# Kernel optimization log

Hardware: AMD Instinct MI355X
Metric: run time of the kernel (lower is better)

The kernel has to match this reference:

```python
import jax, jax.numpy as jnp
import numpy as np

B, C_IN, IMG, P = 32, 3, 224, 16
D, H, L, F, NCLS = 768, 12, 12, 3072, 1000
NP = IMG // P          # 14 patches per side
S = NP * NP + 1        # 197 tokens (cls + patches)
DH = D // H            # 64 head dim
EPS = 1e-5


def _ln(x, g, b):
    m = jnp.mean(x, axis=-1, keepdims=True)
    v = jnp.mean(jnp.square(x - m), axis=-1, keepdims=True)
    return (x - m) * jax.lax.rsqrt(v + EPS) * g + b


def setup_inputs() -> dict:
    key = jax.random.key(0)
    ks = iter(jax.random.split(key, 32))
    w = lambda shape: jax.random.normal(next(ks), shape, dtype=jnp.float32) * 0.02
    inp = {
        "X": jax.random.normal(next(ks), (B, C_IN, IMG, IMG), dtype=jnp.float32),
        "patch_w": w((D, C_IN, P, P)),
        "patch_b": jnp.zeros((D,), jnp.float32),
        "cls_token": w((1, 1, D)),
        "pos_emb": w((1, S, D)),
        # per-layer stacked params; linear weights stored [in, out]
        "ln1_g": jnp.ones((L, D), jnp.float32), "ln1_b": jnp.zeros((L, D), jnp.float32),
        "Wq": w((L, D, D)), "bq": jnp.zeros((L, D), jnp.float32),
        "Wk": w((L, D, D)), "bk": jnp.zeros((L, D), jnp.float32),
        "Wv": w((L, D, D)), "bv": jnp.zeros((L, D), jnp.float32),
        "Wo": w((L, D, D)), "bo": jnp.zeros((L, D), jnp.float32),
        "ln2_g": jnp.ones((L, D), jnp.float32), "ln2_b": jnp.zeros((L, D), jnp.float32),
        "Wf1": w((L, D, F)), "bf1": jnp.zeros((L, F), jnp.float32),
        "Wf2": w((L, F, D)), "bf2": jnp.zeros((L, D), jnp.float32),
        "lnf_g": jnp.ones((D,), jnp.float32), "lnf_b": jnp.zeros((D,), jnp.float32),
        "head_w": w((D, NCLS)), "head_b": jnp.zeros((NCLS,), jnp.float32),
    }
    return inp


def _vit(X, patch_w, patch_b, cls_token, pos_emb,
         ln1_g, ln1_b, Wq, bq, Wk, bk, Wv, bv, Wo, bo,
         ln2_g, ln2_b, Wf1, bf1, Wf2, bf2, lnf_g, lnf_b, head_w, head_b):
    # patch embed: stride==kernel conv as block-reshape + einsum
    xb = X.reshape(B, C_IN, NP, P, NP, P)
    patches = jnp.einsum('bchpwq,dcpq->bhwd', xb, patch_w).reshape(B, NP * NP, D) + patch_b
    x = jnp.concatenate([jnp.broadcast_to(cls_token, (B, 1, D)), patches], axis=1)
    x = x + pos_emb  # [B, S, D]

    scale = 1.0 / jnp.sqrt(jnp.float32(DH))

    def block(x, p):
        g1, b1, wq, bq_, wk, bk_, wv, bv_, wo, bo_, g2, b2, w1, b1f, w2, b2f = p
        h = _ln(x, g1, b1)
        q = (h @ wq + bq_).reshape(B, S, H, DH)
        k = (h @ wk + bk_).reshape(B, S, H, DH)
        v = (h @ wv + bv_).reshape(B, S, H, DH)
        scores = jnp.einsum('bshd,bthd->bhst', q, k) * scale
        probs = jax.nn.softmax(scores, axis=-1)
        attn = jnp.einsum('bhst,bthd->bshd', probs, v).reshape(B, S, D)
        x = x + attn @ wo + bo_
        h = _ln(x, g2, b2)
        x = x + jax.nn.gelu(h @ w1 + b1f, approximate=False) @ w2 + b2f
        return x, None

    layers = (ln1_g, ln1_b, Wq, bq, Wk, bk, Wv, bv, Wo, bo,
              ln2_g, ln2_b, Wf1, bf1, Wf2, bf2)
    x, _ = jax.lax.scan(block, x, layers)

    x = _ln(x, lnf_g, lnf_b)
    return x[:, 0] @ head_w + head_b  # [B, NCLS]


def reference(X, patch_w, patch_b, cls_token, pos_emb,
              ln1_g, ln1_b, Wq, bq, Wk, bk, Wv, bv, Wo, bo,
              ln2_g, ln2_b, Wf1, bf1, Wf2, bf2, lnf_g, lnf_b, head_w, head_b):
    return _vit(X, patch_w, patch_b, cls_token, pos_emb,
                ln1_g, ln1_b, Wq, bq, Wk, bk, Wv, bv, Wo, bo,
                ln2_g, ln2_b, Wf1, bf1, Wf2, bf2, lnf_g, lnf_b, head_w, head_b)
```

## Files before the change

kernel.cpp:

```cpp
#include <hip/hip_runtime.h>
#include <math.h>

#define Bn 32
#define Sn 197
#define Dn 768
#define Hn 12
#define DHn 64
#define Fn 3072
#define Ln 12
#define NPATCH 196
#define NCLSn 1000
#define MTOK (Bn * Sn)
#define MPAD 6400

typedef __attribute__((ext_vector_type(8))) short short8;
typedef __attribute__((ext_vector_type(4))) float f32x4;

__device__ __forceinline__ unsigned short f2bf(float f) {
  union { float f; unsigned int u; } v; v.f = f;
  unsigned int r = v.u + 0x7fffu + ((v.u >> 16) & 1u);
  return (unsigned short)(r >> 16);
}
__device__ __forceinline__ float bf2f(unsigned short h) {
  union { unsigned int u; float f; } v; v.u = ((unsigned int)h) << 16;
  return v.f;
}

__device__ __forceinline__ void gload16(const unsigned short* g, unsigned short* l) {
  __builtin_amdgcn_global_load_lds(
      (const __attribute__((address_space(1))) unsigned int*)g,
      (__attribute__((address_space(3))) unsigned int*)l, 16, 0, 0);
}

__global__ __launch_bounds__(256) void transpose_cast(
    const float* __restrict__ in, unsigned short* __restrict__ out,
    int rows, int cols) {
  __shared__ float tile[32][33];
  int c0 = blockIdx.x * 32, r0 = blockIdx.y * 32;
  int tx = threadIdx.x, ty = threadIdx.y;
  for (int i = 0; i < 32; i += 8) {
    int r = r0 + ty + i, c = c0 + tx;
    tile[ty + i][tx] = (r < rows && c < cols) ? in[(size_t)r * cols + c] : 0.f;
  }
  __syncthreads();
  for (int i = 0; i < 32; i += 8) {
    int c = c0 + ty + i, r = r0 + tx;
    if (c < cols && r < rows)
      out[(size_t)c * rows + r] = f2bf(tile[tx][ty + i]);
  }
}

__global__ __launch_bounds__(256) void cast_bf(
    const float* __restrict__ in, unsigned short* __restrict__ out, int n) {
  int i = blockIdx.x * 256 + threadIdx.x;
  if (i < n) out[i] = f2bf(in[i]);
}

__global__ __launch_bounds__(256) void im2col_patches(
    const float* __restrict__ X, unsigned short* __restrict__ A) {
  int idx = blockIdx.x * 256 + threadIdx.x;
  if (idx >= NPATCH * Bn * Dn) return;
  int col = idx % Dn, row = idx / Dn;
  int b = row / NPATCH, pi = row % NPATCH;
  int hp = pi / 14, wp = pi % 14;
  int c = col >> 8, r2 = col & 255, p = r2 >> 4, q = r2 & 15;
  A[idx] = f2bf(X[(((size_t)b * 3 + c) * 224 + hp * 16 + p) * 224 + wp * 16 + q]);
}

__global__ __launch_bounds__(256) void init_cls(
    const float* __restrict__ cls_tok, const float* __restrict__ pos_emb,
    float* __restrict__ x) {
  int i = blockIdx.x * 256 + threadIdx.x;
  if (i >= Bn * Dn) return;
  int b = i / Dn, d = i % Dn;
  x[(size_t)b * Sn * Dn + d] = cls_tok[d] + pos_emb[d];
}

__global__ __launch_bounds__(256) void pack_qkv_bias(
    const float* __restrict__ bq, const float* __restrict__ bk,
    const float* __restrict__ bv, float* __restrict__ out) {
  int i = blockIdx.x * 256 + threadIdx.x;
  if (i >= Ln * 3 * Dn) return;
  int l = i / (3 * Dn), r = i % (3 * Dn);
  int which = r / Dn, d = r % Dn;
  const float* src = which == 0 ? bq : (which == 1 ? bk : bv);
  out[i] = src[(size_t)l * Dn + d];
}

__global__ __launch_bounds__(256) void layernorm_k(
    const float* __restrict__ x, int row_stride,
    const float* __restrict__ g, const float* __restrict__ b,
    unsigned short* __restrict__ out) {
  int row = blockIdx.x, t = threadIdx.x;
  const float* xr = x + (size_t)row * row_stride;
  float v0 = xr[t], v1 = xr[t + 256], v2 = xr[t + 512];
  float s = v0 + v1 + v2;
  __shared__ float red[4];
  int lane = t & 63, wid = t >> 6;
  for (int off = 32; off > 0; off >>= 1) s += __shfl_xor(s, off, 64);
  if (lane == 0) red[wid] = s;
  __syncthreads();
  float mean = (red[0] + red[1] + red[2] + red[3]) * (1.f / 768.f);
  __syncthreads();
  float d0 = v0 - mean, d1 = v1 - mean, d2 = v2 - mean;
  float q = d0 * d0 + d1 * d1 + d2 * d2;
  for (int off = 32; off > 0; off >>= 1) q += __shfl_xor(q, off, 64);
  if (lane == 0) red[wid] = q;
  __syncthreads();
  float var = (red[0] + red[1] + red[2] + red[3]) * (1.f / 768.f);
  float rstd = rsqrtf(var + 1e-5f);
  size_t o = (size_t)row * Dn;
  out[o + t]       = f2bf(d0 * rstd * g[t]       + b[t]);
  out[o + t + 256] = f2bf(d1 * rstd * g[t + 256] + b[t + 256]);
  out[o + t + 512] = f2bf(d2 * rstd * g[t + 512] + b[t + 512]);
}

template <int MODE>
__global__ __launch_bounds__(256) void gemm128(
    const unsigned short* __restrict__ A, const unsigned short* __restrict__ Bt,
    const float* __restrict__ bias, const float* __restrict__ res,
    float* __restrict__ Cf, unsigned short* __restrict__ Cb,
    int M, int N, int K, int nbn) {
  __shared__ unsigned short As[128][32];
  __shared__ unsigned short Bs[128][32];
  int nwg = gridDim.x;
  int orig = blockIdx.x;
  int qq = nwg >> 3, rr = nwg & 7;
  int xcd = orig & 7, loc = orig >> 3;
  int wg = (xcd < rr ? xcd * (qq + 1) : rr * (qq + 1) + (xcd - rr) * qq) + loc;
  int mb = wg / nbn, nb = wg % nbn;
  int m0 = mb * 128, n0 = nb * 128;

  int tid = threadIdx.x, wid = tid >> 6, lane = tid & 63;
  int wm = (wid >> 1) * 64, wn = (wid & 1) * 64;
  int lrow = lane & 15, lq = lane >> 4;
  int sr = wid * 16 + (lane >> 2);
  int sc = (lane & 3) * 8;
  const unsigned short* Ap = A + (size_t)(m0 + sr) * K + sc;
  const unsigned short* Bp = Bt + (size_t)(n0 + sr) * K + sc;

  f32x4 acc[4][4] = {};
  for (int k0 = 0; k0 < K; k0 += 32) {
    gload16(Ap, &As[wid * 16][0]);
    gload16(Ap + (size_t)64 * K, &As[64 + wid * 16][0]);
    gload16(Bp, &Bs[wid * 16][0]);
    gload16(Bp + (size_t)64 * K, &Bs[64 + wid * 16][0]);
    Ap += 32; Bp += 32;
    __syncthreads();
    short8 af[4], bfr[4];
#pragma unroll
    for (int tm = 0; tm < 4; tm++)
      af[tm] = *(const short8*)(&As[wm + tm * 16 + lrow][lq * 8]);
#pragma unroll
    for (int tn = 0; tn < 4; tn++)
      bfr[tn] = *(const short8*)(&Bs[wn + tn * 16 + lrow][lq * 8]);
#pragma unroll
    for (int tm = 0; tm < 4; tm++)
#pragma unroll
      for (int tn = 0; tn < 4; tn++)
        acc[tm][tn] = __builtin_amdgcn_mfma_f32_16x16x32_bf16(
            af[tm], bfr[tn], acc[tm][tn], 0, 0, 0);
    __syncthreads();
  }

#pragma unroll
  for (int tm = 0; tm < 4; tm++)
#pragma unroll
    for (int tn = 0; tn < 4; tn++)
#pragma unroll
      for (int r = 0; r < 4; r++) {
        int gm = m0 + wm + tm * 16 + lq * 4 + r;
        int gn = n0 + wn + tn * 16 + lrow;
        if (gm >= M || gn >= N) continue;
        float val = acc[tm][tn][r] + bias[gn];
        if constexpr (MODE == 1) {
          size_t o = (size_t)gm * N + gn;
          Cf[o] = val + res[o];
        } else if constexpr (MODE == 2) {
          float gl = 0.5f * val * (1.f + erff(val * 0.70710678118654752f));
          Cb[(size_t)gm * N + gn] = f2bf(gl);
        } else if constexpr (MODE == 3) {
          int b = gm / NPATCH, pi = gm % NPATCH;
          Cf[((size_t)b * Sn + 1 + pi) * Dn + gn] =
              val + res[(size_t)(1 + pi) * Dn + gn];
        } else if constexpr (MODE == 5) {
          int which = gn / Dn;
          int d = gn - which * Dn;
          int b = gm / Sn, s = gm % Sn;
          int h = d >> 6, dh = d & 63;
          Cb[(size_t)which * MPAD * Dn +
             (((size_t)b * Hn + h) * Sn + s) * DHn + dh] = f2bf(val);
        }
      }
}

template <int MODE>
__global__ __launch_bounds__(256) void gemm64(
    const unsigned short* __restrict__ A, const unsigned short* __restrict__ Bt,
    const float* __restrict__ bias, const float* __restrict__ res,
    float* __restrict__ Cf, unsigned short* __restrict__ Cb,
    int M, int N, int K) {
  __shared__ unsigned short As[64][32];
  __shared__ unsigned short Bs[64][32];
  int m0 = blockIdx.x * 64, n0 = blockIdx.y * 64;
  int tid = threadIdx.x;
  int wid = tid >> 6, lane = tid & 63;
  int wm = (wid >> 1) * 32, wn = (wid & 1) * 32;
  int lrow = lane & 15, lq = lane >> 4;
  int lr = tid >> 2, lseg = (tid & 3) * 8;
  f32x4 acc[2][2] = {};
  for (int k0 = 0; k0 < K; k0 += 32) {
    int gm = m0 + lr;
    uint4 av = (gm < M) ? *(const uint4*)(A + (size_t)gm * K + k0 + lseg)
                        : make_uint4(0, 0, 0, 0);
    int gn = n0 + lr;
    uint4 bv = (gn < N) ? *(const uint4*)(Bt + (size_t)gn * K + k0 + lseg)
                        : make_uint4(0, 0, 0, 0);
    __syncthreads();
    *(uint4*)(&As[lr][lseg]) = av;
    *(uint4*)(&Bs[lr][lseg]) = bv;
    __syncthreads();
    short8 a0 = *(const short8*)(&As[wm + lrow][lq * 8]);
    short8 a1 = *(const short8*)(&As[wm + 16 + lrow][lq * 8]);
    short8 b0 = *(const short8*)(&Bs[wn + lrow][lq * 8]);
    short8 b1 = *(const short8*)(&Bs[wn + 16 + lrow][lq * 8]);
    acc[0][0] = __builtin_amdgcn_mfma_f32_16x16x32_bf16(a0, b0, acc[0][0], 0, 0, 0);
    acc[0][1] = __builtin_amdgcn_mfma_f32_16x16x32_bf16(a0, b1, acc[0][1], 0, 0, 0);
    acc[1][0] = __builtin_amdgcn_mfma_f32_16x16x32_bf16(a1, b0, acc[1][0], 0, 0, 0);
    acc[1][1] = __builtin_amdgcn_mfma_f32_16x16x32_bf16(a1, b1, acc[1][1], 0, 0, 0);
  }
#pragma unroll
  for (int tm = 0; tm < 2; tm++)
#pragma unroll
    for (int tn = 0; tn < 2; tn++)
#pragma unroll
      for (int r = 0; r < 4; r++) {
        int ml = wm + tm * 16 + lq * 4 + r;
        int nl = wn + tn * 16 + lrow;
        int gm = m0 + ml, gn = n0 + nl;
        if (gm >= M || gn >= N) continue;
        float val = acc[tm][tn][r] + bias[gn];
        if constexpr (MODE == 4) {
          Cf[(size_t)gm * N + gn] = val;
        }
      }
}

#define QT 16
#define NKT 13
#define PJ 232
__global__ __launch_bounds__(256) void attn_mfma(
    const unsigned short* __restrict__ q, const unsigned short* __restrict__ k,
    const unsigned short* __restrict__ v, unsigned short* __restrict__ out) {
  int bh = blockIdx.x, b = bh / Hn, h = bh % Hn;
  const unsigned short* qp = q + (size_t)bh * Sn * DHn;
  const unsigned short* kp = k + (size_t)bh * Sn * DHn;
  const unsigned short* vp = v + (size_t)bh * Sn * DHn;
  __shared__ unsigned short Vt[DHn][PJ];
  __shared__ unsigned short Pl[4][QT][PJ];
  int t = threadIdx.x, lane = t & 63, wid = t >> 6;
  int col = lane & 15, quad = lane >> 4;

  for (int i = t; i < Sn * DHn; i += 256) {
    int j = i >> 6, d = i & 63;
    Vt[d][j] = vp[i];
  }
  for (int i = t; i < DHn * (PJ - Sn); i += 256) {
    int d = i / (PJ - Sn), j = Sn + i % (PJ - Sn);
    Vt[d][j] = 0;
  }
  for (int i = lane; i < QT * (PJ - NKT * 16); i += 64) {
    int r = i / (PJ - NKT * 16), c = NKT * 16 + i % (PJ - NKT * 16);
    Pl[wid][r][c] = 0;
  }
  __syncthreads();

  for (int qt = wid; qt < NKT; qt += 4) {
    int q0 = qt * QT;
    int qrow = q0 + col;
    int qc = (qrow < Sn) ? qrow : (Sn - 1);
    short8 qa0 = *(const short8*)(qp + (size_t)qc * DHn + quad * 8);
    short8 qa1 = *(const short8*)(qp + (size_t)qc * DHn + 32 + quad * 8);

    f32x4 sc[NKT];
    for (int kt = 0; kt < NKT; kt++) {
      int krow = kt * QT + col;
      int kc = (krow < Sn) ? krow : (Sn - 1);
      short8 kb0 = *(const short8*)(kp + (size_t)kc * DHn + quad * 8);
      short8 kb1 = *(const short8*)(kp + (size_t)kc * DHn + 32 + quad * 8);
      f32x4 c = {};
      c = __builtin_amdgcn_mfma_f32_16x16x32_bf16(qa0, kb0, c, 0, 0, 0);
      c = __builtin_amdgcn_mfma_f32_16x16x32_bf16(qa1, kb1, c, 0, 0, 0);
      if (krow >= Sn)
        for (int r = 0; r < 4; r++) c[r] = -1e30f;
      sc[kt] = c;
    }

    for (int r = 0; r < 4; r++) {
      float m = -1e30f;
      for (int kt = 0; kt < NKT; kt++) m = fmaxf(m, sc[kt][r]);
      for (int off = 1; off < 16; off <<= 1) m = fmaxf(m, __shfl_xor(m, off, 64));
      float s = 0.f;
      for (int kt = 0; kt < NKT; kt++) {
        float e = __expf((sc[kt][r] - m) * 0.125f);
        sc[kt][r] = e;
        s += e;
      }
      for (int off = 1; off < 16; off <<= 1) s += __shfl_xor(s, off, 64);
      float inv = 1.f / s;
      int row = quad * 4 + r;
      for (int kt = 0; kt < NKT; kt++)
        Pl[wid][row][kt * 16 + col] = f2bf(sc[kt][r] * inv);
    }

    f32x4 o[4] = {};
    for (int jc = 0; jc < 7; jc++) {
      short8 pa = *(const short8*)(&Pl[wid][col][jc * 32 + quad * 8]);
      for (int dt = 0; dt < 4; dt++) {
        short8 vb = *(const short8*)(&Vt[dt * 16 + col][jc * 32 + quad * 8]);
        o[dt] = __builtin_amdgcn_mfma_f32_16x16x32_bf16(pa, vb, o[dt], 0, 0, 0);
      }
    }

    for (int dt = 0; dt < 4; dt++)
      for (int r = 0; r < 4; r++) {
        int qq = q0 + quad * 4 + r;
        if (qq < Sn)
          out[((size_t)b * Sn + qq) * Dn + h * DHn + dt * 16 + col] =
              f2bf(o[dt][r]);
      }
  }
}

extern "C" void kernel_launch(void* const* d_in, const int* in_sizes, int n_in,
                              void* d_out, int out_size, void* d_ws, size_t ws_size,
                              hipStream_t stream) {
  const float* X       = (const float*)d_in[0];
  const float* patch_w = (const float*)d_in[1];
  const float* patch_b = (const float*)d_in[2];
  const float* cls_tok = (const float*)d_in[3];
  const float* pos_emb = (const float*)d_in[4];
  const float* ln1_g = (const float*)d_in[5];
  const float* ln1_b = (const float*)d_in[6];
  const float* Wq = (const float*)d_in[7];
  const float* bq = (const float*)d_in[8];
  const float* Wk = (const float*)d_in[9];
  const float* bk = (const float*)d_in[10];
  const float* Wv = (const float*)d_in[11];
  const float* bv = (const float*)d_in[12];
  const float* Wo = (const float*)d_in[13];
  const float* bo = (const float*)d_in[14];
  const float* ln2_g = (const float*)d_in[15];
  const float* ln2_b = (const float*)d_in[16];
  const float* Wf1 = (const float*)d_in[17];
  const float* bf1 = (const float*)d_in[18];
  const float* Wf2 = (const float*)d_in[19];
  const float* bf2 = (const float*)d_in[20];
  const float* lnf_g = (const float*)d_in[21];
  const float* lnf_b = (const float*)d_in[22];
  const float* head_w = (const float*)d_in[23];
  const float* head_b = (const float*)d_in[24];
  float* out = (float*)d_out;

  char* base = (char*)d_ws;
  size_t off = 0;
  auto alloc = [&](size_t bytes) -> void* {
    void* p = base + off;
    off += (bytes + 255) & ~(size_t)255;
    return p;
  };
  unsigned short* wq_t  = (unsigned short*)alloc((size_t)Dn * Dn * 2);
  unsigned short* wk_t  = (unsigned short*)alloc((size_t)Dn * Dn * 2);
  unsigned short* wv_t  = (unsigned short*)alloc((size_t)Dn * Dn * 2);
  unsigned short* wo_t  = (unsigned short*)alloc((size_t)Dn * Dn * 2);
  unsigned short* wf1_t = (unsigned short*)alloc((size_t)Dn * Fn * 2);
  unsigned short* wf2_t = (unsigned short*)alloc((size_t)Dn * Fn * 2);
  unsigned short* pw_bf = (unsigned short*)alloc((size_t)Dn * Dn * 2);
  unsigned short* hw_t  = (unsigned short*)alloc((size_t)NCLSn * Dn * 2);
  unsigned short* im2c  = (unsigned short*)alloc((size_t)MPAD * Dn * 2);
  float*          x     = (float*)alloc((size_t)MTOK * Dn * 4);
  unsigned short* h_bf  = (unsigned short*)alloc((size_t)MPAD * Dn * 2);
  unsigned short* qb    = (unsigned short*)alloc((size_t)MPAD * Dn * 2);
  unsigned short* kb    = (unsigned short*)alloc((size_t)MPAD * Dn * 2);
  unsigned short* vb    = (unsigned short*)alloc((size_t)MPAD * Dn * 2);
  unsigned short* atob  = (unsigned short*)alloc((size_t)MPAD * Dn * 2);
  unsigned short* gel   = (unsigned short*)alloc((size_t)MPAD * Fn * 2);
  unsigned short* clsb  = (unsigned short*)alloc((size_t)Bn * Dn * 2);
  float*          bqkv  = (float*)alloc((size_t)Ln * 3 * Dn * 4);
  (void)ws_size; (void)in_sizes; (void)n_in; (void)out_size;

  dim3 tb(32, 8);
  auto tgrid = [](int rows, int cols) { return dim3((cols + 31) / 32, (rows + 31) / 32); };
  auto g128 = [](int M, int N) {
    return dim3((unsigned)(((M + 127) / 128) * ((N + 127) / 128)));
  };

  cast_bf<<<(Dn * Dn + 255) / 256, 256, 0, stream>>>(patch_w, pw_bf, Dn * Dn);
  transpose_cast<<<tgrid(Dn, NCLSn), tb, 0, stream>>>(head_w, hw_t, Dn, NCLSn);
  pack_qkv_bias<<<(Ln * 3 * Dn + 255) / 256, 256, 0, stream>>>(bq, bk, bv, bqkv);
  im2col_patches<<<(Bn * NPATCH * Dn + 255) / 256, 256, 0, stream>>>(X, im2c);
  init_cls<<<(Bn * Dn + 255) / 256, 256, 0, stream>>>(cls_tok, pos_emb, x);
  gemm128<3><<<g128(Bn * NPATCH, Dn), 256, 0, stream>>>(
      im2c, pw_bf, patch_b, pos_emb, x, nullptr, Bn * NPATCH, Dn, Dn, Dn / 128);

  for (int l = 0; l < Ln; l++) {
    const size_t wo_off = (size_t)l * Dn * Dn;
    const size_t wf_off = (size_t)l * Dn * Fn;
    transpose_cast<<<tgrid(Dn, Dn), tb, 0, stream>>>(Wq + wo_off, wq_t, Dn, Dn);
    transpose_cast<<<tgrid(Dn, Dn), tb, 0, stream>>>(Wk + wo_off, wk_t, Dn, Dn);
    transpose_cast<<<tgrid(Dn, Dn), tb, 0, stream>>>(Wv + wo_off, wv_t, Dn, Dn);
    transpose_cast<<<tgrid(Dn, Dn), tb, 0, stream>>>(Wo + wo_off, wo_t, Dn, Dn);
    transpose_cast<<<tgrid(Dn, Fn), tb, 0, stream>>>(Wf1 + wf_off, wf1_t, Dn, Fn);
    transpose_cast<<<tgrid(Fn, Dn), tb, 0, stream>>>(Wf2 + wf_off, wf2_t, Fn, Dn);

    layernorm_k<<<MTOK, 256, 0, stream>>>(x, Dn, ln1_g + (size_t)l * Dn,
                                          ln1_b + (size_t)l * Dn, h_bf);
    gemm128<5><<<g128(MTOK, 3 * Dn), 256, 0, stream>>>(
        h_bf, wq_t, bqkv + (size_t)l * 3 * Dn, nullptr, nullptr, qb,
        MTOK, 3 * Dn, Dn, 3 * Dn / 128);
    attn_mfma<<<Bn * Hn, 256, 0, stream>>>(qb, kb, vb, atob);
    gemm128<1><<<g128(MTOK, Dn), 256, 0, stream>>>(
        atob, wo_t, bo + (size_t)l * Dn, x, x, nullptr, MTOK, Dn, Dn, Dn / 128);
    layernorm_k<<<MTOK, 256, 0, stream>>>(x, Dn, ln2_g + (size_t)l * Dn,
                                          ln2_b + (size_t)l * Dn, h_bf);
    gemm128<2><<<g128(MTOK, Fn), 256, 0, stream>>>(
        h_bf, wf1_t, bf1 + (size_t)l * Fn, nullptr, nullptr, gel,
        MTOK, Fn, Dn, Fn / 128);
    gemm128<1><<<g128(MTOK, Dn), 256, 0, stream>>>(
        gel, wf2_t, bf2 + (size_t)l * Dn, x, x, nullptr, MTOK, Dn, Fn, Dn / 128);
  }

  layernorm_k<<<Bn, 256, 0, stream>>>(x, Sn * Dn, lnf_g, lnf_b, clsb);
  gemm64<4><<<dim3(1, (NCLSn + 63) / 64), 256, 0, stream>>>(
      clsb, hw_t, head_b, nullptr, out, nullptr, Bn, NCLSn, Dn);
}
```

Measured before the change: 4.359 ms.

## Hoist weight transposes into batched launches and split-K the narrow output GEMMs

All per-layer weight transpose/cast work is moved out of the layer loop into six batched launches (grid z over layers), writing into preallocated per-layer bf16 buffers when workspace allows. The Wo and FFN2 projections (N=768, few 128x128 tiles) are split along K into 2 and 4 chunks that write fp32 partials, followed by a reduce kernel that adds bias and residual. This targets under-filled grids on the narrow GEMMs and many small launches. In exchange it adds partial-sum traffic of up to 4 fp32 copies of the activation per FFN2, plus an extra kernel per projection, and needs more workspace.

```diff
diff --git a/kernel.cpp b/kernel.cpp
--- a/kernel.cpp
+++ b/kernel.cpp
@@ -47,6 +47,27 @@
     int c = c0 + ty + i, r = r0 + tx;
     if (c < cols && r < rows)
       out[(size_t)c * rows + r] = f2bf(tile[tx][ty + i]);
+  }
+}
+
+__global__ __launch_bounds__(256) void transpose_cast_b(
+    const float* __restrict__ in, unsigned short* __restrict__ out,
+    int rows, int cols, size_t in_ls, size_t out_ls, int coff) {
+  __shared__ float tile[32][33];
+  int l = blockIdx.z;
+  in += (size_t)l * in_ls;
+  out += (size_t)l * out_ls;
+  int c0 = blockIdx.x * 32, r0 = blockIdx.y * 32;
+  int tx = threadIdx.x, ty = threadIdx.y;
+  for (int i = 0; i < 32; i += 8) {
+    int r = r0 + ty + i, c = c0 + tx;
+    tile[ty + i][tx] = (r < rows && c < cols) ? in[(size_t)r * cols + c] : 0.f;
+  }
+  __syncthreads();
+  for (int i = 0; i < 32; i += 8) {
+    int c = c0 + ty + i, r = r0 + tx;
+    if (c < cols && r < rows)
+      out[(size_t)(c + coff) * rows + r] = f2bf(tile[tx][ty + i]);
   }
 }
 
@@ -115,12 +136,28 @@
   out[o + t + 512] = f2bf(d2 * rstd * g[t + 512] + b[t + 512]);
 }
 
+__global__ __launch_bounds__(256) void splitk_reduce(
+    const float* __restrict__ part, const float* __restrict__ bias,
+    float* __restrict__ x, int N, int ks) {
+  size_t e = ((size_t)blockIdx.x * 256 + threadIdx.x) * 4;
+  if (e >= (size_t)MTOK * N) return;
+  f32x4 s = *(const f32x4*)(x + e);
+  int gn = (int)(e % N);
+  const float* bp = bias + gn;
+  s[0] += bp[0]; s[1] += bp[1]; s[2] += bp[2]; s[3] += bp[3];
+  for (int kc = 0; kc < ks; kc++) {
+    f32x4 p = *(const f32x4*)(part + (size_t)kc * MTOK * N + e);
+    s[0] += p[0]; s[1] += p[1]; s[2] += p[2]; s[3] += p[3];
+  }
+  *(f32x4*)(x + e) = s;
+}
+
 template <int MODE>
 __global__ __launch_bounds__(256) void gemm128(
     const unsigned short* __restrict__ A, const unsigned short* __restrict__ Bt,
     const float* __restrict__ bias, const float* __restrict__ res,
     float* __restrict__ Cf, unsigned short* __restrict__ Cb,
-    int M, int N, int K, int nbn) {
+    int M, int N, int KC, int kstride, int ksplit, int nbn) {
   __shared__ unsigned short As[128][32];
   __shared__ unsigned short Bs[128][32];
   int nwg = gridDim.x;
@@ -128,7 +165,10 @@
   int qq = nwg >> 3, rr = nwg & 7;
   int xcd = orig & 7, loc = orig >> 3;
   int wg = (xcd < rr ? xcd * (qq + 1) : rr * (qq + 1) + (xcd - rr) * qq) + loc;
-  int mb = wg / nbn, nb = wg % nbn;
+  int ntiles = nwg / ksplit;
+  int kc = wg / ntiles;
+  int tile = wg - kc * ntiles;
+  int mb = tile / nbn, nb = tile % nbn;
   int m0 = mb * 128, n0 = nb * 128;
 
   int tid = threadIdx.x, wid = tid >> 6, lane = tid & 63;
@@ -136,15 +176,15 @@
   int lrow = lane & 15, lq = lane >> 4;
   int sr = wid * 16 + (lane >> 2);
   int sc = (lane & 3) * 8;
-  const unsigned short* Ap = A + (size_t)(m0 + sr) * K + sc;
-  const unsigned short* Bp = Bt + (size_t)(n0 + sr) * K + sc;
+  const unsigned short* Ap = A + (size_t)(m0 + sr) * kstride + (size_t)kc * KC + sc;
+  const unsigned short* Bp = Bt + (size_t)(n0 + sr) * kstride + (size_t)kc * KC + sc;
 
   f32x4 acc[4][4] = {};
-  for (int k0 = 0; k0 < K; k0 += 32) {
+  for (int k0 = 0; k0 < KC; k0 += 32) {
     gload16(Ap, &As[wid * 16][0]);
-    gload16(Ap + (size_t)64 * K, &As[64 + wid * 16][0]);
+    gload16(Ap + (size_t)64 * kstride, &As[64 + wid * 16][0]);
     gload16(Bp, &Bs[wid * 16][0]);
-    gload16(Bp + (size_t)64 * K, &Bs[64 + wid * 16][0]);
+    gload16(Bp + (size_t)64 * kstride, &Bs[64 + wid * 16][0]);
     Ap += 32; Bp += 32;
     __syncthreads();
     short8 af[4], bfr[4];
@@ -172,7 +212,9 @@
         int gm = m0 + wm + tm * 16 + lq * 4 + r;
         int gn = n0 + wn + tn * 16 + lrow;
         if (gm >= M || gn >= N) continue;
-        float val = acc[tm][tn][r] + bias[gn];
+        float val;
+        if constexpr (MODE == 6) val = acc[tm][tn][r];
+        else val = acc[tm][tn][r] + bias[gn];
         if constexpr (MODE == 1) {
           size_t o = (size_t)gm * N + gn;
           Cf[o] = val + res[o];
@@ -190,6 +232,8 @@
           int h = d >> 6, dh = d & 63;
           Cb[(size_t)which * MPAD * Dn +
              (((size_t)b * Hn + h) * Sn + s) * DHn + dh] = f2bf(val);
+        } else if constexpr (MODE == 6) {
+          Cf[((size_t)kc * MTOK + gm) * N + gn] = val;
         }
       }
 }
@@ -387,12 +431,29 @@
   unsigned short* gel   = (unsigned short*)alloc((size_t)MPAD * Fn * 2);
   unsigned short* clsb  = (unsigned short*)alloc((size_t)Bn * Dn * 2);
   float*          bqkv  = (float*)alloc((size_t)Ln * 3 * Dn * 4);
-  (void)ws_size; (void)in_sizes; (void)n_in; (void)out_size;
+  (void)in_sizes; (void)n_in; (void)out_size;
+
+  const size_t SZ_PART = (size_t)4 * MTOK * Dn * 4;
+  float* part = nullptr;
+  if (off + SZ_PART + 4096 <= ws_size) part = (float*)alloc(SZ_PART);
+  const size_t SZ_QKV = (size_t)Ln * 3 * Dn * Dn * 2;
+  const size_t SZ_WO  = (size_t)Ln * Dn * Dn * 2;
+  const size_t SZ_WF  = (size_t)Ln * Dn * Fn * 2;
+  unsigned short *wqkv_all = nullptr, *wo_all = nullptr,
+                 *wf1_all = nullptr, *wf2_all = nullptr;
+  if (off + SZ_QKV + SZ_WO + 2 * SZ_WF + 8192 <= ws_size) {
+    wqkv_all = (unsigned short*)alloc(SZ_QKV);
+    wo_all   = (unsigned short*)alloc(SZ_WO);
+    wf1_all  = (unsigned short*)alloc(SZ_WF);
+    wf2_all  = (unsigned short*)alloc(SZ_WF);
+  }
+  const bool sk = part != nullptr;
+  const bool hoist = wqkv_all != nullptr;
 
   dim3 tb(32, 8);
   auto tgrid = [](int rows, int cols) { return dim3((cols + 31) / 32, (rows + 31) / 32); };
-  auto g128 = [](int M, int N) {
-    return dim3((unsigned)(((M + 127) / 128) * ((N + 127) / 128)));
+  auto g128 = [](int M, int N, int ks) {
+    return dim3((unsigned)(((M + 127) / 128) * ((N + 127) / 128) * ks));
   };
 
   cast_bf<<<(Dn * Dn + 255) / 256, 256, 0, stream>>>(patch_w, pw_bf, Dn * Dn);
@@ -400,34 +461,72 @@
   pack_qkv_bias<<<(Ln * 3 * Dn + 255) / 256, 256, 0, stream>>>(bq, bk, bv, bqkv);
   im2col_patches<<<(Bn * NPATCH * Dn + 255) / 256, 256, 0, stream>>>(X, im2c);
   init_cls<<<(Bn * Dn + 255) / 256, 256, 0, stream>>>(cls_tok, pos_emb, x);
-  gemm128<3><<<g128(Bn * NPATCH, Dn), 256, 0, stream>>>(
-      im2c, pw_bf, patch_b, pos_emb, x, nullptr, Bn * NPATCH, Dn, Dn, Dn / 128);
+  gemm128<3><<<g128(Bn * NPATCH, Dn, 1), 256, 0, stream>>>(
+      im2c, pw_bf, patch_b, pos_emb, x, nullptr, Bn * NPATCH, Dn, Dn, Dn, 1, Dn / 128);
+
+  if (hoist) {
+    dim3 z88(24, 24, Ln);
+    transpose_cast_b<<<z88, tb, 0, stream>>>(
+        Wq, wqkv_all, Dn, Dn, (size_t)Dn * Dn, (size_t)3 * Dn * Dn, 0);
+    transpose_cast_b<<<z88, tb, 0, stream>>>(
+        Wk, wqkv_all, Dn, Dn, (size_t)Dn * Dn, (size_t)3 * Dn * Dn, Dn);
+    transpose_cast_b<<<z88, tb, 0, stream>>>(
+        Wv, wqkv_all, Dn, Dn, (size_t)Dn * Dn, (size_t)3 * Dn * Dn, 2 * Dn);
+    transpose_cast_b<<<z88, tb, 0, stream>>>(
+        Wo, wo_all, Dn, Dn, (size_t)Dn * Dn, (size_t)Dn * Dn, 0);
+    transpose_cast_b<<<dim3(96, 24, Ln), tb, 0, stream>>>(
+        Wf1, wf1_all, Dn, Fn, (size_t)Dn * Fn, (size_t)Fn * Dn, 0);
+    transpose_cast_b<<<dim3(24, 96, Ln), tb, 0, stream>>>(
+        Wf2, wf2_all, Fn, Dn, (size_t)Fn * Dn, (size_t)Dn * Fn, 0);
+  }
 
   for (int l = 0; l < Ln; l++) {
     const size_t wo_off = (size_t)l * Dn * Dn;
     const size_t wf_off = (size_t)l * Dn * Fn;
-    transpose_cast<<<tgrid(Dn, Dn), tb, 0, stream>>>(Wq + wo_off, wq_t, Dn, Dn);
-    transpose_cast<<<tgrid(Dn, Dn), tb, 0, stream>>>(Wk + wo_off, wk_t, Dn, Dn);
-    transpose_cast<<<tgrid(Dn, Dn), tb, 0, stream>>>(Wv + wo_off, wv_t, Dn, Dn);
-    transpose_cast<<<tgrid(Dn, Dn), tb, 0, stream>>>(Wo + wo_off, wo_t, Dn, Dn);
-    transpose_cast<<<tgrid(Dn, Fn), tb, 0, stream>>>(Wf1 + wf_off, wf1_t, Dn, Fn);
-    transpose_cast<<<tgrid(Fn, Dn), tb, 0, stream>>>(Wf2 + wf_off, wf2_t, Fn, Dn);
+    const unsigned short* wqkv_l = hoist ? wqkv_all + (size_t)l * 3 * Dn * Dn : wq_t;
+    const unsigned short* wo_l   = hoist ? wo_all + wo_off : wo_t;
+    const unsigned short* wf1_l  = hoist ? wf1_all + wf_off : wf1_t;
+    const unsigned short* wf2_l  = hoist ? wf2_all + wf_off : wf2_t;
+    if (!hoist) {
+      transpose_cast<<<tgrid(Dn, Dn), tb, 0, stream>>>(Wq + wo_off, wq_t, Dn, Dn);
+      transpose_cast<<<tgrid(Dn, Dn), tb, 0, stream>>>(Wk + wo_off, wk_t, Dn, Dn);
+      transpose_cast<<<tgrid(Dn, Dn), tb, 0, stream>>>(Wv + wo_off, wv_t, Dn, Dn);
+      transpose_cast<<<tgrid(Dn, Dn), tb, 0, stream>>>(Wo + wo_off, wo_t, Dn, Dn);
+      transpose_cast<<<tgrid(Dn, Fn), tb, 0, stream>>>(Wf1 + wf_off, wf1_t, Dn, Fn);
+      transpose_cast<<<tgrid(Fn, Dn), tb, 0, stream>>>(Wf2 + wf_off, wf2_t, Fn, Dn);
+    }
 
     layernorm_k<<<MTOK, 256, 0, stream>>>(x, Dn, ln1_g + (size_t)l * Dn,
                                           ln1_b + (size_t)l * Dn, h_bf);
-    gemm128<5><<<g128(MTOK, 3 * Dn), 256, 0, stream>>>(
-        h_bf, wq_t, bqkv + (size_t)l * 3 * Dn, nullptr, nullptr, qb,
-        MTOK, 3 * Dn, Dn, 3 * Dn / 128);
+    gemm128<5><<<g128(MTOK, 3 * Dn, 1), 256, 0, stream>>>(
+        h_bf, wqkv_l, bqkv + (size_t)l * 3 * Dn, nullptr, nullptr, qb,
+        MTOK, 3 * Dn, Dn, Dn, 1, 3 * Dn / 128);
     attn_mfma<<<Bn * Hn, 256, 0, stream>>>(qb, kb, vb, atob);
-    gemm128<1><<<g128(MTOK, Dn), 256, 0, stream>>>(
-        atob, wo_t, bo + (size_t)l * Dn, x, x, nullptr, MTOK, Dn, Dn, Dn / 128);
+    if (sk) {
+      gemm128<6><<<g128(MTOK, Dn, 2), 256, 0, stream>>>(
+          atob, wo_l, nullptr, nullptr, part, nullptr,
+          MTOK, Dn, Dn / 2, Dn, 2, Dn / 128);
+      splitk_reduce<<<(MTOK * Dn / 4 + 255) / 256, 256, 0, stream>>>(
+          part, bo + (size_t)l * Dn, x, Dn, 2);
+    } else {
+      gemm128<1><<<g128(MTOK, Dn, 1), 256, 0, stream>>>(
+          atob, wo_l, bo + (size_t)l * Dn, x, x, nullptr, MTOK, Dn, Dn, Dn, 1, Dn / 128);
+    }
     layernorm_k<<<MTOK, 256, 0, stream>>>(x, Dn, ln2_g + (size_t)l * Dn,
                                           ln2_b + (size_t)l * Dn, h_bf);
-    gemm128<2><<<g128(MTOK, Fn), 256, 0, stream>>>(
-        h_bf, wf1_t, bf1 + (size_t)l * Fn, nullptr, nullptr, gel,
-        MTOK, Fn, Dn, Fn / 128);
-    gemm128<1><<<g128(MTOK, Dn), 256, 0, stream>>>(
-        gel, wf2_t, bf2 + (size_t)l * Dn, x, x, nullptr, MTOK, Dn, Fn, Dn / 128);
+    gemm128<2><<<g128(MTOK, Fn, 1), 256, 0, stream>>>(
+        h_bf, wf1_l, bf1 + (size_t)l * Fn, nullptr, nullptr, gel,
+        MTOK, Fn, Dn, Dn, 1, Fn / 128);
+    if (sk) {
+      gemm128<6><<<g128(MTOK, Dn, 4), 256, 0, stream>>>(
+          gel, wf2_l, nullptr, nullptr, part, nullptr,
+          MTOK, Dn, Fn / 4, Fn, 4, Dn / 128);
+      splitk_reduce<<<(MTOK * Dn / 4 + 255) / 256, 256, 0, stream>>>(
+          part, bf2 + (size_t)l * Dn, x, Dn, 4);
+    } else {
+      gemm128<1><<<g128(MTOK, Dn, 1), 256, 0, stream>>>(
+          gel, wf2_l, bf2 + (size_t)l * Dn, x, x, nullptr, MTOK, Dn, Fn, Fn, 1, Dn / 128);
+    }
   }
 
   layernorm_k<<<Bn, 256, 0, stream>>>(x, Sn * Dn, lnf_g, lnf_b, clsb);
```

After: 3.935 ms. -9.7%, faster.
